# Optimization experiments

Measured on AMD Instinct MI355X. Metric: run time of the kernel, lower is better.

Reference implementation:

```python
import jax, jax.numpy as jnp
import numpy as np

THRESH = 0.5
LENS = 0.5
DECAY = 0.5
IN_SIZE = 8
T = 784 // IN_SIZE  # 98 timesteps
H = 1024
OUT = 10
SKIP = (2, 3, 4)
N_BATCH = 1024


@jax.custom_vjp
def act_fun(x):
    return (x > THRESH).astype(x.dtype)

def _af_fwd(x):
    return act_fun(x), x

def _af_bwd(x, g):
    return (g * (jnp.abs(x - THRESH) < LENS).astype(g.dtype),)

act_fun.defvjp(_af_fwd, _af_bwd)


def _make_mask(dim, cycle):
    base = np.array([1 if t % cycle == 0 else 0 for t in range(T)], dtype=np.int32)
    return np.stack([np.roll(base, n) for n in range(dim)])  # [dim, T]


def setup_inputs() -> dict:
    key = jax.random.key(0)
    ks = jax.random.split(key, 9)
    inp = {
        "input": jax.random.uniform(ks[0], (N_BATCH, 784), dtype=jnp.float32),
        "W1": jax.random.normal(ks[1], (H, IN_SIZE), dtype=jnp.float32) * 0.1,
        "b1": jax.random.normal(ks[2], (H,), dtype=jnp.float32) * 0.01,
        "W2": jax.random.normal(ks[3], (H, H), dtype=jnp.float32) * 0.03,
        "b2": jax.random.normal(ks[4], (H,), dtype=jnp.float32) * 0.01,
        "W3": jax.random.normal(ks[5], (H, H), dtype=jnp.float32) * 0.03,
        "b3": jax.random.normal(ks[6], (H,), dtype=jnp.float32) * 0.01,
        "W4": jax.random.normal(ks[7], (OUT, H), dtype=jnp.float32) * 0.03,
        "b4": jax.random.normal(ks[8], (OUT,), dtype=jnp.float32) * 0.01,
        "mask1": jnp.asarray(_make_mask(H, SKIP[0])),
        "mask2": jnp.asarray(_make_mask(H, SKIP[1])),
        "mask3": jnp.asarray(_make_mask(H, SKIP[2])),
    }
    return inp


def _gather_steps(x):
    # Faithful replication of the original (buggy) slicing: start = step*IN_SIZE,
    # but if start >= T - IN_SIZE the model uses the LAST IN_SIZE pixels.
    starts = np.array([s * IN_SIZE if s * IN_SIZE < T - IN_SIZE else 784 - IN_SIZE
                       for s in range(T)])
    idx = starts[:, None] + np.arange(IN_SIZE)  # [T, IN_SIZE]
    return jnp.transpose(x[:, idx], (1, 0, 2))  # [T, N, IN_SIZE]


def reference(input, W1, b1, W2, b2, W3, b3, W4, b4, mask1, mask2, mask3):
    N = input.shape[0]
    xs = _gather_steps(input)            # [T, N, IN_SIZE]
    mk1 = mask1.T                         # [T, H]
    mk2 = mask2.T
    mk3 = mask3.T

    def upd(drive, mem, spike, mk):
        mkf = mk.astype(mem.dtype)
        new_mem = mem * DECAY * (1.0 - spike) + drive
        mem = jnp.where(mk == 0, mem, new_mem)
        spike = act_fun(mem) * mkf
        return mem, spike

    zeros = lambda d: jnp.zeros((N, d), dtype=input.dtype)
    carry0 = (zeros(H), zeros(H), zeros(H), zeros(H), zeros(H), zeros(H),
              jnp.zeros((N, OUT), dtype=input.dtype), zeros(H), zeros(H), zeros(H))

    def step(carry, inp):
        m1, s1, m2, s2, m3, s3, osum, ss1, ss2, ss3 = carry
        x, k1, k2, k3 = inp
        m1, s1 = upd(x @ W1.T + b1, m1, s1, k1)
        m2, s2 = upd(s1 @ W2.T + b2, m2, s2, k2)
        m3, s3 = upd(s2 @ W3.T + b3, m3, s3, k3)
        out = s3 @ W4.T + b4
        return (m1, s1, m2, s2, m3, s3, osum + out,
                ss1 + s1, ss2 + s2, ss3 + s3), None

    carry, _ = jax.lax.scan(step, carry0, (xs, mk1, mk2, mk3))
    _, _, _, _, _, _, osum, ss1, ss2, ss3 = carry

    tw = jnp.asarray(T, dtype=input.dtype)
    outputs = osum / tw
    denom = jnp.asarray(N * H * T, dtype=input.dtype)
    layer_fr = jnp.stack([ss1.sum() / denom, ss2.sum() / denom, ss3.sum() / denom])
    hidden_spk = (ss1 / tw, ss2 / tw, ss3 / tw)
    return outputs, hidden_spk, layer_fr
```

## Files before the change

kernel.cpp:

```cpp
#include <hip/hip_runtime.h>

#define TTL 98
#define OUTD 10

typedef float f16v __attribute__((ext_vector_type(16)));
typedef short short8 __attribute__((ext_vector_type(8)));
typedef unsigned long ul2 __attribute__((ext_vector_type(2)));
typedef unsigned short ushort;

constexpr size_t MM = 1048576;
constexpr size_t OFF_OSUM = 5 * MM;
constexpr size_t OFF_XT   = OFF_OSUM + 10240;
constexpr size_t OFF_S1B  = OFF_XT + 802816;
constexpr size_t OFF_S2B  = OFF_S1B + 1605632;
constexpr size_t OFF_S1BT = OFF_S2B + 1103872;
constexpr size_t OFF_S2BT = OFF_S1BT + 1605632;
constexpr size_t OFF_W2S  = OFF_S2BT + 1103872;
constexpr size_t OFF_W3S  = OFF_W2S + 1572864;
constexpr size_t FIX_END  = OFF_W3S + 1585152;

constexpr size_t TAB_IDX2 = 0;
constexpr size_t TAB_IDX3 = 37632;
constexpr size_t TAB_CQ3  = 269696;
constexpr size_t TAB_L2   = 304192;
constexpr size_t TAB_L3   = 337984;

constexpr size_t AW3_PER_T = 168960;

__device__ inline void split3(float w, ushort& h, ushort& m, ushort& l) {
    unsigned u = __float_as_uint(w);
    h = (ushort)(u >> 16);
    float r1 = w - __uint_as_float(u & 0xFFFF0000u);
    unsigned u1 = __float_as_uint(r1);
    m = (ushort)(u1 >> 16);
    float r2 = r1 - __uint_as_float(u1 & 0xFFFF0000u);
    l = (ushort)(__float_as_uint(r2) >> 16);
}

__device__ inline short8 expand8(unsigned x) {
    union { unsigned u[4]; short8 v; } r;
#pragma unroll
    for (int q = 0; q < 4; ++q) {
        unsigned b = x >> (2 * q);
        r.u[q] = ((b & 1u) * 0x3F80u) | ((b & 2u) ? 0x3F800000u : 0u);
    }
    return r.v;
}

__device__ inline short8 ldsAF(const ushort* base) {
    union { unsigned long u[2]; short8 s; } r;
    r.u[0] = *(const unsigned long*)(base);
    r.u[1] = *(const unsigned long*)(base + 4);
    return r.s;
}
__device__ inline void ldsWR(ushort* dst, ul2 v) {
    *(unsigned long*)(dst) = v[0];
    *(unsigned long*)(dst + 4) = v[1];
}
#define ASOFF(cur, pi, row, col) (((((cur)*3 + (pi))*64 + (row))*36) + (col))

__global__ __launch_bounds__(256) void kSplit(
    const float* __restrict__ W2, const float* __restrict__ W3,
    ushort* __restrict__ W2S, ushort* __restrict__ W3S)
{
    int id = blockIdx.x * 256 + threadIdx.x;
    if (id < 1048576) {
        int p = id >> 19, rem = id & 524287, i = rem >> 9, q = rem & 511;
        ushort h, m, l;
        split3(W2[i * 1024 + 2 * q + p], h, m, l);
        size_t base = (size_t)p * 524288 + (size_t)i * 512 + q;
        W2S[base] = h; W2S[base + 1048576] = m; W2S[base + 2097152] = l;
    } else {
        int id2 = id - 1048576;
        if (id2 >= 1056768) return;
        int c = id2 / 352256, rem = id2 % 352256, i = rem / 344, q = rem % 344;
        int j = c + 3 * q;
        float w = (j < 1024) ? W3[i * 1024 + j] : 0.f;
        ushort h, m, l;
        split3(w, h, m, l);
        W3S[id2] = h; W3S[id2 + 1056768] = m; W3S[id2 + 2113536] = l;
    }
}

__global__ __launch_bounds__(256) void kPrep(const float* __restrict__ input,
                                             float* __restrict__ xT)
{
    __shared__ float Ls[64][65];
    int bx = blockIdx.x, tid = threadIdx.x;
    int wt = bx >> 4, nt = bx & 15;
    int w0 = wt * 64, n0 = nt * 64;
#pragma unroll
    for (int j = 0; j < 16; ++j) {
        int flat = tid + 256 * j;
        int a = flat >> 6, c = flat & 63;
        Ls[a][c] = (w0 + c < 784) ? input[(size_t)(n0 + a) * 784 + w0 + c] : 0.f;
    }
    __syncthreads();
#pragma unroll
    for (int j = 0; j < 16; ++j) {
        int flat = tid + 256 * j;
        int ii = flat >> 6, nn = flat & 63;
        if (w0 + ii < 784) xT[(size_t)(w0 + ii) * 1024 + n0 + nn] = Ls[nn][ii];
    }
}

__global__ __launch_bounds__(256) void kL1(
    const float* __restrict__ xT, const float* __restrict__ W1,
    const float* __restrict__ b1,
    unsigned long long* __restrict__ s1bits, float* __restrict__ ss1)
{
    int tid = threadIdx.x;
    int waveId = (blockIdx.x << 2) + (tid >> 6);
    int lane = tid & 63;
    int rowg = waveId >> 4;
    int nblk = waveId & 15;
    int i0 = rowg << 2;
    int n = (nblk << 6) + lane;
    float w[4][8], bb[4], mem[4], cnt[4];
#pragma unroll
    for (int r = 0; r < 4; ++r) {
#pragma unroll
        for (int e = 0; e < 8; ++e) w[r][e] = W1[(i0 + r) * 8 + e];
        bb[r] = b1[i0 + r]; mem[r] = 0.f; cnt[r] = 0.f;
    }
    float x[8], xn[8];
#pragma unroll
    for (int e = 0; e < 8; ++e) x[e] = xT[(size_t)e * 1024 + n];
    for (int t = 0; t < 12; ++t) {
        int st1 = ((t + 1) * 8 < TTL - 8) ? (t + 1) * 8 : (784 - 8);
#pragma unroll
        for (int e = 0; e < 8; ++e) xn[e] = xT[(size_t)(st1 + e) * 1024 + n];
#pragma unroll
        for (int r = 0; r < 4; ++r) {
            if (((t ^ (i0 + r)) & 1) == 0) {
                float d = bb[r];
#pragma unroll
                for (int e = 0; e < 8; ++e) d += w[r][e] * x[e];
                float m = mem[r] * 0.5f + d;
                mem[r] = m;
                bool sp = m > 0.5f;
                unsigned long long bm = __ballot(sp);
                if (lane == 0) s1bits[(size_t)(t * 512 + ((i0 + r) >> 1)) * 16 + nblk] = bm;
                if (sp) cnt[r] += 1.f;
            }
        }
#pragma unroll
        for (int e = 0; e < 8; ++e) x[e] = xn[e];
    }
    float dd[4];
#pragma unroll
    for (int r = 0; r < 4; ++r) {
        float d = bb[r];
#pragma unroll
        for (int e = 0; e < 8; ++e) d += w[r][e] * x[e];
        dd[r] = d;
    }
#pragma unroll 1
    for (int t = 12; t < TTL; t += 2) {
#pragma unroll
        for (int h = 0; h < 2; ++h) {
#pragma unroll
            for (int rr = 0; rr < 2; ++rr) {
                int r = h + rr * 2;
                float m = mem[r] * 0.5f + dd[r];
                mem[r] = m;
                bool sp = m > 0.5f;
                unsigned long long bm = __ballot(sp);
                if (lane == 0) s1bits[(size_t)((t + h) * 512 + ((i0 + r) >> 1)) * 16 + nblk] = bm;
                if (sp) cnt[r] += 1.f;
            }
        }
    }
#pragma unroll
    for (int r = 0; r < 4; ++r) ss1[(size_t)(i0 + r) * 1024 + n] = cnt[r];
}

__global__ __launch_bounds__(256) void kTab2(
    int* __restrict__ idx2, int* __restrict__ idx3, int* __restrict__ cq3)
{
    __shared__ int f2[256], f3[256];
    __shared__ int sidx2[384], sidx3[320];
    int t = blockIdx.x, tid = threadIdx.x;
    int a2[4], a3[4];
    int l2 = 0, l3 = 0;
#pragma unroll
    for (int e = 0; e < 4; ++e) {
        int i = tid * 4 + e;
        int u = (t - i) % TTL; if (u < 0) u += TTL;
        a2[e] = (u % 3 == 0); a3[e] = (u % 4 == 0);
        l2 += a2[e]; l3 += a3[e];
    }
    f2[tid] = l2; f3[tid] = l3;
    __syncthreads();
    for (int s = 1; s < 256; s <<= 1) {
        int v2 = (tid >= s) ? f2[tid - s] : 0;
        int v3 = (tid >= s) ? f3[tid - s] : 0;
        __syncthreads();
        f2[tid] += v2; f3[tid] += v3;
        __syncthreads();
    }
    int o2 = f2[tid] - l2, o3 = f3[tid] - l3;
    int c2 = f2[255], c3 = f3[255];
#pragma unroll
    for (int e = 0; e < 4; ++e) {
        int i = tid * 4 + e;
        if (a2[e]) { sidx2[o2] = i; ++o2; }
        if (a3[e]) { sidx3[o3] = i; ++o3; }
    }
    __syncthreads();
    for (int k = tid; k < 384; k += 256) idx2[t * 384 + k] = (k < c2) ? sidx2[k] : -1;
    for (int k = tid; k < 320; k += 256) idx3[t * 320 + k] = (k < c3) ? sidx3[k] : -1;
    for (int k = tid; k < 352; k += 256) {
        int j = (k < c2) ? sidx2[k] : 0;
        cq3[t * 352 + k] = (j % 3) * 352256 + j / 3;
    }
}

template<int C, int NACT>
__global__ __launch_bounds__(256) void kListCF(int* __restrict__ list)
{
    int flat = blockIdx.x * 256 + threadIdx.x;
    if (flat >= 1024 * NACT) return;
    int i = flat / NACT, s = flat % NACT;
    int ri = i % 98;
    int k0 = (98 - ri + C - 1) / C;
    int kw = NACT - k0; if (kw < 0) kw = 0;
    int t = (s < kw) ? (ri + (k0 + s) * C - 98) : (ri + (s - kw) * C);
    int rk = 0;
    int r = t;
#pragma unroll
    for (int k = 0; k < NACT; ++k) {
        rk += (r < i) ? (i - r + 97) / 98 : 0;
        r -= C; if (r < 0) r += 98;
    }
    list[i * NACT + s] = (t << 10) | rk;
}

template<int K>
__global__ __launch_bounds__(256) void kXb(const unsigned* __restrict__ in,
                                           unsigned* __restrict__ out, int t0)
{
    constexpr int Kw = K / 32;
    __shared__ unsigned L[1024];
    int bx = blockIdx.x, tid = threadIdx.x;
    int tt = t0 + bx / Kw, kw = bx % Kw;
    const unsigned* ip = in + ((size_t)tt * K + kw * 32) * 32;
#pragma unroll
    for (int g = 0; g < 4; ++g) L[g * 256 + tid] = ip[g * 256 + tid];
    __syncthreads();
    unsigned* op = out + ((size_t)tt * Kw + kw) * 1024;
#pragma unroll
    for (int g = 0; g < 4; ++g) {
        int n = g * 256 + tid;
        int w = n >> 5, b = n & 31;
        unsigned acc = 0;
#pragma unroll
        for (int k = 0; k < 32; ++k) acc |= ((L[k * 32 + w] >> b) & 1u) << k;
        op[n] = acc;
    }
}

__global__ __launch_bounds__(256) void kXbG3A(
    const unsigned* __restrict__ s2b, unsigned* __restrict__ s2bT,
    const ushort* __restrict__ Ws, const int* __restrict__ idx3,
    const int* __restrict__ cq3, ushort* __restrict__ AW3, int t0)
{
    __shared__ unsigned L[1024];
    int bx = blockIdx.x, tid = threadIdx.x;
    int tloc = bx / 66, r66 = bx % 66;
    int t = t0 + tloc;
    if (r66 < 11) {
        int kw = r66;
        const unsigned* ip = s2b + ((size_t)t * 352 + kw * 32) * 32;
#pragma unroll
        for (int g = 0; g < 4; ++g) L[g * 256 + tid] = ip[g * 256 + tid];
        __syncthreads();
        unsigned* op = s2bT + ((size_t)t * 11 + kw) * 1024;
#pragma unroll
        for (int g = 0; g < 4; ++g) {
            int n = g * 256 + tid;
            int w = n >> 5, b = n & 31;
            unsigned acc = 0;
#pragma unroll
            for (int k = 0; k < 32; ++k) acc |= ((L[k * 32 + w] >> b) & 1u) << k;
            op[n] = acc;
        }
    } else {
        int blk = r66 - 11;
        int flat = blk * 256 + tid;
        int r = flat / 44, kg = flat % 44;
        int k0 = kg * 8;
        int v = idx3[t * 320 + r];
        int i = v < 0 ? 0 : v;
        const int* cq = cq3 + t * 352 + k0;
        int c0 = cq[0], c1 = cq[1], c2 = cq[2], c3 = cq[3],
            c4 = cq[4], c5 = cq[5], c6 = cq[6], c7 = cq[7];
        size_t ia = (size_t)i * 344;
#pragma unroll
        for (int pi = 0; pi < 3; ++pi) {
            const ushort* wp = Ws + (size_t)pi * 1056768 + ia;
            union { ushort us[8]; ul2 v2; } o;
            o.us[0] = wp[c0]; o.us[1] = wp[c1]; o.us[2] = wp[c2]; o.us[3] = wp[c3];
            o.us[4] = wp[c4]; o.us[5] = wp[c5]; o.us[6] = wp[c6]; o.us[7] = wp[c7];
            *(ul2*)(AW3 + ((size_t)tloc * 3 + pi) * 112640 + (size_t)r * 352 + k0) = o.v2;
        }
    }
}


__device__ __forceinline__ void gm2_body(
    int bx, int tid, ushort* AsR,
    const ushort* __restrict__ Ws, const unsigned* __restrict__ s1bT,
    const int* __restrict__ idx2, float* __restrict__ drive, int t0)
{
    int tloc = bx / 24, rem = bx % 24;
    int mt = rem >> 2, nt4 = rem & 3;
    int t = t0 + tloc;
    int p = t & 1;
    int r0 = mt * 64, n0 = nt4 * 256;
    int ar = tid >> 2, ak8 = (tid & 3) * 8;
    int vR = idx2[t * 384 + r0 + ar];
    const ushort* Wrow = Ws + (size_t)p * 524288 + (size_t)(vR < 0 ? 0 : vR) * 512 + ak8;
    int wv = tid >> 6, lane = tid & 63;
    int mrow = lane & 31, kh8 = (lane >> 5) * 8;
    int nb = n0 + wv * 64 + mrow;
    f16v acc[2][2];
#pragma unroll
    for (int a = 0; a < 2; ++a)
#pragma unroll
        for (int b = 0; b < 2; ++b) acc[a][b] = (f16v)(0.f);

    ul2 c0r[3];
#pragma unroll
    for (int pi = 0; pi < 3; ++pi) c0r[pi] = *(const ul2*)(Wrow + (size_t)pi * 1048576);
#pragma unroll
    for (int pi = 0; pi < 3; ++pi) ldsWR(&AsR[ASOFF(0, pi, ar, ak8)], c0r[pi]);
    ul2 nxt[3];
#pragma unroll
    for (int pi = 0; pi < 3; ++pi) nxt[pi] = *(const ul2*)(Wrow + (size_t)pi * 1048576 + 32);
    unsigned w4c[2];
#pragma unroll
    for (int jj = 0; jj < 2; ++jj) w4c[jj] = s1bT[(size_t)t * 16 * 1024 + nb + jj * 32];
    __syncthreads();

    int cur = 0;
    for (int kc = 0; kc < 512; kc += 32) {
        if (kc + 32 < 512) {
#pragma unroll
            for (int pi = 0; pi < 3; ++pi) ldsWR(&AsR[ASOFF(cur ^ 1, pi, ar, ak8)], nxt[pi]);
        }
        unsigned w4n[2];
        if (kc + 32 < 512) {
#pragma unroll
            for (int jj = 0; jj < 2; ++jj)
                w4n[jj] = s1bT[((size_t)t * 16 + ((kc + 32) >> 5)) * 1024 + nb + jj * 32];
        }
        ul2 n2[3];
        if (kc + 64 < 512) {
#pragma unroll
            for (int pi = 0; pi < 3; ++pi)
                n2[pi] = *(const ul2*)(Wrow + (size_t)pi * 1048576 + kc + 64);
        }
#pragma unroll
        for (int s2 = 0; s2 < 2; ++s2) {
            int kcol = s2 * 16 + kh8;
            short8 bf[2];
#pragma unroll
            for (int jj = 0; jj < 2; ++jj) bf[jj] = expand8((w4c[jj] >> kcol) & 0xFFu);
#pragma unroll
            for (int wr2 = 0; wr2 < 2; ++wr2) {
                short8 af0 = ldsAF(&AsR[ASOFF(cur, 0, wr2 * 32 + mrow, kcol)]);
                short8 af1 = ldsAF(&AsR[ASOFF(cur, 1, wr2 * 32 + mrow, kcol)]);
                short8 af2 = ldsAF(&AsR[ASOFF(cur, 2, wr2 * 32 + mrow, kcol)]);
#pragma unroll
                for (int jj = 0; jj < 2; ++jj) {
                    acc[wr2][jj] = __builtin_amdgcn_mfma_f32_32x32x16_bf16(af2, bf[jj], acc[wr2][jj], 0, 0, 0);
                    acc[wr2][jj] = __builtin_amdgcn_mfma_f32_32x32x16_bf16(af1, bf[jj], acc[wr2][jj], 0, 0, 0);
                    acc[wr2][jj] = __builtin_amdgcn_mfma_f32_32x32x16_bf16(af0, bf[jj], acc[wr2][jj], 0, 0, 0);
                }
            }
        }
        __syncthreads();
        cur ^= 1;
        nxt[0] = n2[0]; nxt[1] = n2[1]; nxt[2] = n2[2];
        w4c[0] = w4n[0]; w4c[1] = w4n[1];
    }
#pragma unroll
    for (int wr2 = 0; wr2 < 2; ++wr2)
#pragma unroll
        for (int jj = 0; jj < 2; ++jj)
#pragma unroll
            for (int reg = 0; reg < 16; ++reg) {
                int rowl = r0 + wr2 * 32 + (reg & 3) + 8 * (reg >> 2) + 4 * (lane >> 5);
                drive[((size_t)tloc * 384 + rowl) * 1024 + nb + jj * 32] = acc[wr2][jj][reg];
            }
}

__device__ __forceinline__ void gm3_body(
    int bx, int tid, ushort* AsR,
    const ushort* __restrict__ AW3, const unsigned* __restrict__ s2bT,
    float* __restrict__ drive, int t0)
{
    int tloc = bx / 20, rem = bx % 20;
    int mt = rem >> 2, nt4 = rem & 3;
    int t = t0 + tloc;
    int r0 = mt * 64, n0 = nt4 * 256;
    int ar = tid >> 2, ak8 = (tid & 3) * 8;
    const ushort* Ab = AW3 + (size_t)tloc * 337920 + (size_t)(r0 + ar) * 352 + ak8;
    int wv = tid >> 6, lane = tid & 63;
    int mrow = lane & 31, kh8 = (lane >> 5) * 8;
    int nb = n0 + wv * 64 + mrow;
    f16v acc[2][2];
#pragma unroll
    for (int a = 0; a < 2; ++a)
#pragma unroll
        for (int b = 0; b < 2; ++b) acc[a][b] = (f16v)(0.f);

    ul2 c0r[3];
#pragma unroll
    for (int pi = 0; pi < 3; ++pi) c0r[pi] = *(const ul2*)(Ab + (size_t)pi * 112640);
#pragma unroll
    for (int pi = 0; pi < 3; ++pi) ldsWR(&AsR[ASOFF(0, pi, ar, ak8)], c0r[pi]);
    ul2 nxt[3];
#pragma unroll
    for (int pi = 0; pi < 3; ++pi) nxt[pi] = *(const ul2*)(Ab + (size_t)pi * 112640 + 32);
    unsigned w4c[2];
#pragma unroll
    for (int jj = 0; jj < 2; ++jj) w4c[jj] = s2bT[(size_t)t * 11 * 1024 + nb + jj * 32];
    __syncthreads();

    int cur = 0;
    for (int kc = 0; kc < 352; kc += 32) {
        if (kc + 32 < 352) {
#pragma unroll
            for (int pi = 0; pi < 3; ++pi) ldsWR(&AsR[ASOFF(cur ^ 1, pi, ar, ak8)], nxt[pi]);
        }
        unsigned w4n[2];
        if (kc + 32 < 352) {
#pragma unroll
            for (int jj = 0; jj < 2; ++jj)
                w4n[jj] = s2bT[((size_t)t * 11 + ((kc + 32) >> 5)) * 1024 + nb + jj * 32];
        }
        ul2 n2[3];
        if (kc + 64 < 352) {
#pragma unroll
            for (int pi = 0; pi < 3; ++pi)
                n2[pi] = *(const ul2*)(Ab + (size_t)pi * 112640 + kc + 64);
        }
#pragma unroll
        for (int s2 = 0; s2 < 2; ++s2) {
            int kcol = s2 * 16 + kh8;
            short8 bf[2];
#pragma unroll
            for (int jj = 0; jj < 2; ++jj) bf[jj] = expand8((w4c[jj] >> kcol) & 0xFFu);
#pragma unroll
            for (int wr2 = 0; wr2 < 2; ++wr2) {
                short8 af0 = ldsAF(&AsR[ASOFF(cur, 0, wr2 * 32 + mrow, kcol)]);
                short8 af1 = ldsAF(&AsR[ASOFF(cur, 1, wr2 * 32 + mrow, kcol)]);
                short8 af2 = ldsAF(&AsR[ASOFF(cur, 2, wr2 * 32 + mrow, kcol)]);
#pragma unroll
                for (int jj = 0; jj < 2; ++jj) {
                    acc[wr2][jj] = __builtin_amdgcn_mfma_f32_32x32x16_bf16(af2, bf[jj], acc[wr2][jj], 0, 0, 0);
                    acc[wr2][jj] = __builtin_amdgcn_mfma_f32_32x32x16_bf16(af1, bf[jj], acc[wr2][jj], 0, 0, 0);
                    acc[wr2][jj] = __builtin_amdgcn_mfma_f32_32x32x16_bf16(af0, bf[jj], acc[wr2][jj], 0, 0, 0);
                }
            }
        }
        __syncthreads();
        cur ^= 1;
        nxt[0] = n2[0]; nxt[1] = n2[1]; nxt[2] = n2[2];
        w4c[0] = w4n[0]; w4c[1] = w4n[1];
    }
#pragma unroll
    for (int wr2 = 0; wr2 < 2; ++wr2)
#pragma unroll
        for (int jj = 0; jj < 2; ++jj)
#pragma unroll
            for (int reg = 0; reg < 16; ++reg) {
                int rowl = r0 + wr2 * 32 + (reg & 3) + 8 * (reg >> 2) + 4 * (lane >> 5);
                drive[((size_t)tloc * 320 + rowl) * 1024 + nb + jj * 32] = acc[wr2][jj][reg];
            }
}

__global__ __launch_bounds__(256) void kGM2K(
    const ushort* __restrict__ Ws, const unsigned* __restrict__ s1bT,
    const int* __restrict__ idx2, float* __restrict__ drive, int t0)
{
    __shared__ ushort AsR[2 * 3 * 64 * 36];
    gm2_body(blockIdx.x, threadIdx.x, AsR, Ws, s1bT, idx2, drive, t0);
}
__global__ __launch_bounds__(256) void kGM3K(
    const ushort* __restrict__ AW3, const unsigned* __restrict__ s2bT,
    float* __restrict__ drive, int t0)
{
    __shared__ ushort AsR[2 * 3 * 64 * 36];
    gm3_body(blockIdx.x, threadIdx.x, AsR, AW3, s2bT, drive, t0);
}

__global__ __launch_bounds__(256) void kGMF(
    const ushort* __restrict__ W2S, const unsigned* __restrict__ s1bT,
    const int* __restrict__ idx2, float* __restrict__ drv2, int t0_2, int n2blocks,
    const ushort* __restrict__ AW3, const unsigned* __restrict__ s2bT,
    float* __restrict__ drv3, int t0_3)
{
    __shared__ ushort AsR[2 * 3 * 64 * 36];
    int bx = blockIdx.x;
    if (bx < n2blocks) gm2_body(bx, threadIdx.x, AsR, W2S, s1bT, idx2, drv2, t0_2);
    else               gm3_body(bx - n2blocks, threadIdx.x, AsR, AW3, s2bT, drv3, t0_3);
}

template<int MP, int KBP, bool BITS, int NACT>
__device__ __forceinline__ void rk_body(
    int bx, int tid,
    const float* __restrict__ drive, const float* __restrict__ bias,
    const int* __restrict__ list,
    float* __restrict__ mG, float* __restrict__ ssG,
    unsigned long long* __restrict__ bitsOut, int t0, int nt)
{
    int row = bx >> 2;
    int wv  = ((bx & 3) << 2) + (tid >> 6);
    int lane = tid & 63;
    int n = (wv << 6) + lane;
    size_t idx = (size_t)row * 1024 + n;
    float mv = mG[idx];
    float cnt = 0.f;
    float bv = bias[row];
    const int* lp = list + row * NACT;
    int t1 = t0 + nt;
    int s0 = 0;
    while (s0 < NACT && (lp[s0] >> 10) < t0) ++s0;
    int s1 = s0;
    while (s1 < NACT && (lp[s1] >> 10) < t1) ++s1;
    if (s0 < s1) {
        int v0 = lp[s0];
        float d0 = drive[((size_t)((v0 >> 10) - t0) * MP + (v0 & 1023)) * 1024 + n];
        int v1 = 0; float d1 = 0.f;
        if (s0 + 1 < s1) {
            v1 = lp[s0 + 1];
            d1 = drive[((size_t)((v1 >> 10) - t0) * MP + (v1 & 1023)) * 1024 + n];
        }
        for (int s = s0; s < s1; ++s) {
            int vc = v0;
            float dcur = d0;
            v0 = v1; d0 = d1;
            if (s + 2 < s1) {
                v1 = lp[s + 2];
                d1 = drive[((size_t)((v1 >> 10) - t0) * MP + (v1 & 1023)) * 1024 + n];
            }
            float d = dcur + bv;
            float m = mv * 0.5f + d;
            mv = m;
            bool sp = m > 0.5f;
            if (BITS) {
                unsigned long long bm = __ballot(sp);
                if (lane == 0) bitsOut[((size_t)(vc >> 10) * KBP + (vc & 1023)) * 16 + wv] = bm;
            }
            cnt += sp ? 1.f : 0.f;
        }
    }
    mG[idx] = mv;
    ssG[idx] += cnt;
}

template<int MP, int KBP, bool BITS, int NACT>
__global__ __launch_bounds__(256) void kRK(
    const float* __restrict__ drive, const float* __restrict__ bias,
    const int* __restrict__ list,
    float* __restrict__ mG, float* __restrict__ ssG,
    unsigned long long* __restrict__ bitsOut, int t0, int nt)
{
    rk_body<MP, KBP, BITS, NACT>(blockIdx.x, threadIdx.x, drive, bias, list,
                                 mG, ssG, bitsOut, t0, nt);
}

__global__ __launch_bounds__(256) void kRKF(
    const float* __restrict__ drv3, const float* __restrict__ b3,
    const int* __restrict__ list3, float* __restrict__ m3, float* __restrict__ ss3,
    int t0_3, int nt3,
    const float* __restrict__ drv2, const float* __restrict__ b2,
    const int* __restrict__ list2, float* __restrict__ m2, float* __restrict__ ss2,
    unsigned long long* __restrict__ s2bits, int t0_2, int nt2)
{
    int bx = blockIdx.x;
    if (bx < 4096)
        rk_body<320, 0, false, 25>(bx, threadIdx.x, drv3, b3, list3, m3, ss3,
                                   nullptr, t0_3, nt3);
    else
        rk_body<384, 352, true, 33>(bx - 4096, threadIdx.x, drv2, b2, list2, m2, ss2,
                                    s2bits, t0_2, nt2);
}

__global__ __launch_bounds__(256) void kTail(
    const float* __restrict__ ssBase, const float* __restrict__ W4,
    float* __restrict__ osum, float* __restrict__ out, float* __restrict__ fr)
{
    int bx = blockIdx.x, tid = threadIdx.x;
    if (bx < 768) {
        __shared__ float Ls[64][65];
        __shared__ float red[4];
        int l = bx >> 8;
        int tile = bx & 255;
        int i0 = (tile >> 4) * 64, n0 = (tile & 15) * 64;
        const float* ss = ssBase + (size_t)l * MM;
        float* o = out + 10240 + (size_t)l * MM;
        float sum = 0.f;
#pragma unroll
        for (int j = 0; j < 16; ++j) {
            int flat = tid + 256 * j;
            int a = flat >> 6, c = flat & 63;
            float v = ss[(size_t)(i0 + a) * 1024 + n0 + c];
            Ls[a][c] = v;
            sum += v;
        }
        __syncthreads();
        for (int off = 32; off > 0; off >>= 1) sum += __shfl_down(sum, off, 64);
        if ((tid & 63) == 0) red[tid >> 6] = sum;
        __syncthreads();
        if (tid == 0) {
            float s = red[0] + red[1] + red[2] + red[3];
            atomicAdd(&fr[l], s * (1.0f / (1024.0f * 1024.0f * 98.0f)));
        }
#pragma unroll
        for (int j = 0; j < 16; ++j) {
            int flat = tid + 256 * j;
            int nn = flat >> 6, ii = flat & 63;
            o[(size_t)(n0 + nn) * 1024 + i0 + ii] = Ls[ii][nn] * (1.0f / 98.0f);
        }
    } else {
        int b = bx - 768;
        int ks = b >> 4, nt = b & 15;
        int n = nt * 64 + (tid & 63);
        int og = tid >> 6;
        const float* ss3 = ssBase + (size_t)2 * MM;
        float a0 = 0.f, a1 = 0.f, a2 = 0.f;
        int k0 = ks * 256;
        for (int k = k0; k < k0 + 256; ++k) {
            float v = ss3[(size_t)k * 1024 + n];
            a0 += v * W4[og * 1024 + k];
            a1 += v * W4[(og + 4) * 1024 + k];
            if (og < 2) a2 += v * W4[(og + 8) * 1024 + k];
        }
        atomicAdd(&osum[n * OUTD + og], a0);
        atomicAdd(&osum[n * OUTD + og + 4], a1);
        if (og < 2) atomicAdd(&osum[n * OUTD + og + 8], a2);
    }
}

__global__ void kOut(const float* __restrict__ osum, const float* __restrict__ b4,
                     float* __restrict__ out)
{
    int idx = blockIdx.x * 256 + threadIdx.x;
    if (idx < 1024 * OUTD) out[idx] = osum[idx] * (1.0f / 98.0f) + b4[idx % OUTD];
}

extern "C" void kernel_launch(void* const* d_in, const int* in_sizes, int n_in,
                              void* d_out, int out_size, void* d_ws, size_t ws_size,
                              hipStream_t stream)
{
    const float* input = (const float*)d_in[0];
    const float* W1    = (const float*)d_in[1];
    const float* b1    = (const float*)d_in[2];
    const float* W2    = (const float*)d_in[3];
    const float* b2    = (const float*)d_in[4];
    const float* W3    = (const float*)d_in[5];
    const float* b3    = (const float*)d_in[6];
    const float* W4    = (const float*)d_in[7];
    const float* b4    = (const float*)d_in[8];

    float* ws = (float*)d_ws;
    float* ss1  = ws;
    float* ss2  = ws + MM;
    float* ss3  = ws + 2 * MM;
    float* m2   = ws + 3 * MM;
    float* m3   = ws + 4 * MM;
    float* osum = ws + OFF_OSUM;
    float* xT   = ws + OFF_XT;
    int*   tabs = (int*)(ws + OFF_XT);
    int* idx2  = tabs + TAB_IDX2;
    int* idx3  = tabs + TAB_IDX3;
    int* cq3   = tabs + TAB_CQ3;
    int* list2 = tabs + TAB_L2;
    int* list3 = tabs + TAB_L3;
    unsigned int* s1b  = (unsigned int*)(ws + OFF_S1B);
    unsigned int* s2b  = (unsigned int*)(ws + OFF_S2B);
    unsigned int* s1bT = (unsigned int*)(ws + OFF_S1BT);
    unsigned int* s2bT = (unsigned int*)(ws + OFF_S2BT);
    ushort* W2S = (ushort*)(ws + OFF_W2S);
    ushort* W3S = (ushort*)(ws + OFF_W3S);
    float* out  = (float*)d_out;

    size_t availF = ws_size / sizeof(float);
    constexpr size_t PER_T = AW3_PER_T + 384 * 1024 + 320 * 1024;
    int tc = 10;
    const int cands[8] = {98, 66, 49, 40, 33, 25, 14, 10};
    for (int ci = 0; ci < 8; ++ci) {
        if (FIX_END + (size_t)cands[ci] * PER_T <= availF) { tc = cands[ci]; break; }
    }
    ushort* AW3 = (ushort*)(ws + FIX_END);
    float* drv2 = ws + FIX_END + (size_t)tc * AW3_PER_T;
    float* drv3 = drv2 + (size_t)tc * 384 * 1024;

    hipMemsetAsync(ws, 0, (5 * MM + 10240) * sizeof(float), stream);
    hipMemsetAsync(s2b, 0, 1103872 * sizeof(unsigned int), stream);
    hipMemsetAsync(out + 3155968, 0, 3 * sizeof(float), stream);

    kSplit<<<8224, 256, 0, stream>>>(W2, W3, W2S, W3S);
    kPrep<<<208, 256, 0, stream>>>(input, xT);
    kL1<<<1024, 256, 0, stream>>>(xT, W1, b1, (unsigned long long*)s1b, ss1);
    kTab2<<<98, 256, 0, stream>>>(idx2, idx3, cq3);
    kListCF<3, 33><<<132, 256, 0, stream>>>(list2);
    kListCF<4, 25><<<100, 256, 0, stream>>>(list3);
    kXb<512><<<1568, 256, 0, stream>>>(s1b, s1bT, 0);

    int nc = (TTL + tc - 1) / tc;
    auto ntOf = [&](int c) { int t0c = c * tc; return (TTL - t0c < tc) ? (TTL - t0c) : tc; };

    kGM2K<<<ntOf(0) * 24, 256, 0, stream>>>(W2S, s1bT, idx2, drv2, 0);
    kRK<384, 352, true, 33><<<4096, 256, 0, stream>>>(drv2, b2, list2, m2, ss2,
                                                      (unsigned long long*)s2b, 0, ntOf(0));
    kXbG3A<<<ntOf(0) * 66, 256, 0, stream>>>(s2b, s2bT, W3S, idx3, cq3, AW3, 0);

    for (int c = 0; c + 1 < nc; ++c) {
        int t03 = c * tc, t02 = (c + 1) * tc;
        int n2b = ntOf(c + 1) * 24, n3b = ntOf(c) * 20;
        kGMF<<<n2b + n3b, 256, 0, stream>>>(W2S, s1bT, idx2, drv2, t02, n2b,
                                            AW3, s2bT, drv3, t03);
        kRKF<<<8192, 256, 0, stream>>>(drv3, b3, list3, m3, ss3, t03, ntOf(c),
                                       drv2, b2, list2, m2, ss2,
                                       (unsigned long long*)s2b, t02, ntOf(c + 1));
        kXbG3A<<<ntOf(c + 1) * 66, 256, 0, stream>>>(s2b, s2bT, W3S, idx3, cq3, AW3, t02);
    }
    int cl = nc - 1, t0l = cl * tc;
    kGM3K<<<ntOf(cl) * 20, 256, 0, stream>>>(AW3, s2bT, drv3, t0l);
    kRK<320, 0, false, 25><<<4096, 256, 0, stream>>>(drv3, b3, list3, m3, ss3,
                                                     nullptr, t0l, ntOf(cl));

    kTail<<<832, 256, 0, stream>>>(ss1, W4, osum, out, out + 3155968);
    kOut<<<40, 256, 0, stream>>>(osum, b4, out);
}
```

Measured before the change: 518.7 us.

## Load MFMA A-fragments directly from global memory, dropping LDS staging

The two spiking-layer GEMM bodies no longer stage the weight (A) tiles through double-buffered shared memory with a __syncthreads per K-chunk. Each lane now loads its own MFMA A fragments straight from global memory into registers and prefetches the next chunk. This removes the LDS traffic, the barriers and the LDS footprint, which may raise occupancy. In exchange, the four waves of a block each reload the same A rows (4x global/L2 traffic), and register pressure rises from holding 24 short8 fragments.

```diff
diff --git a/kernel.cpp b/kernel.cpp
--- a/kernel.cpp
+++ b/kernel.cpp
@@ -46,18 +46,6 @@
     }
     return r.v;
 }
-
-__device__ inline short8 ldsAF(const ushort* base) {
-    union { unsigned long u[2]; short8 s; } r;
-    r.u[0] = *(const unsigned long*)(base);
-    r.u[1] = *(const unsigned long*)(base + 4);
-    return r.s;
-}
-__device__ inline void ldsWR(ushort* dst, ul2 v) {
-    *(unsigned long*)(dst) = v[0];
-    *(unsigned long*)(dst + 4) = v[1];
-}
-#define ASOFF(cur, pi, row, col) (((((cur)*3 + (pi))*64 + (row))*36) + (col))
 
 __global__ __launch_bounds__(256) void kSplit(
     const float* __restrict__ W2, const float* __restrict__ W3,
@@ -309,7 +297,7 @@
 
 
 __device__ __forceinline__ void gm2_body(
-    int bx, int tid, ushort* AsR,
+    int bx, int tid,
     const ushort* __restrict__ Ws, const unsigned* __restrict__ s1bT,
     const int* __restrict__ idx2, float* __restrict__ drive, int t0)
 {
@@ -318,48 +306,47 @@
     int t = t0 + tloc;
     int p = t & 1;
     int r0 = mt * 64, n0 = nt4 * 256;
-    int ar = tid >> 2, ak8 = (tid & 3) * 8;
-    int vR = idx2[t * 384 + r0 + ar];
-    const ushort* Wrow = Ws + (size_t)p * 524288 + (size_t)(vR < 0 ? 0 : vR) * 512 + ak8;
     int wv = tid >> 6, lane = tid & 63;
     int mrow = lane & 31, kh8 = (lane >> 5) * 8;
     int nb = n0 + wv * 64 + mrow;
+    int vR0 = idx2[t * 384 + r0 + mrow];
+    int vR1 = idx2[t * 384 + r0 + 32 + mrow];
+    const ushort* Ar[2];
+    Ar[0] = Ws + (size_t)p * 524288 + (size_t)(vR0 < 0 ? 0 : vR0) * 512 + kh8;
+    Ar[1] = Ws + (size_t)p * 524288 + (size_t)(vR1 < 0 ? 0 : vR1) * 512 + kh8;
     f16v acc[2][2];
 #pragma unroll
     for (int a = 0; a < 2; ++a)
 #pragma unroll
         for (int b = 0; b < 2; ++b) acc[a][b] = (f16v)(0.f);
 
-    ul2 c0r[3];
-#pragma unroll
-    for (int pi = 0; pi < 3; ++pi) c0r[pi] = *(const ul2*)(Wrow + (size_t)pi * 1048576);
-#pragma unroll
-    for (int pi = 0; pi < 3; ++pi) ldsWR(&AsR[ASOFF(0, pi, ar, ak8)], c0r[pi]);
-    ul2 nxt[3];
-#pragma unroll
-    for (int pi = 0; pi < 3; ++pi) nxt[pi] = *(const ul2*)(Wrow + (size_t)pi * 1048576 + 32);
+    short8 fc[2][2][3];
+#pragma unroll
+    for (int s2 = 0; s2 < 2; ++s2)
+#pragma unroll
+        for (int wr2 = 0; wr2 < 2; ++wr2)
+#pragma unroll
+            for (int pi = 0; pi < 3; ++pi)
+                fc[s2][wr2][pi] = *(const short8*)(Ar[wr2] + (size_t)pi * 1048576 + s2 * 16);
     unsigned w4c[2];
 #pragma unroll
     for (int jj = 0; jj < 2; ++jj) w4c[jj] = s1bT[(size_t)t * 16 * 1024 + nb + jj * 32];
-    __syncthreads();
-
-    int cur = 0;
+
+#pragma unroll 1
     for (int kc = 0; kc < 512; kc += 32) {
-        if (kc + 32 < 512) {
-#pragma unroll
-            for (int pi = 0; pi < 3; ++pi) ldsWR(&AsR[ASOFF(cur ^ 1, pi, ar, ak8)], nxt[pi]);
-        }
+        short8 fn[2][2][3];
         unsigned w4n[2];
         if (kc + 32 < 512) {
 #pragma unroll
+            for (int s2 = 0; s2 < 2; ++s2)
+#pragma unroll
+                for (int wr2 = 0; wr2 < 2; ++wr2)
+#pragma unroll
+                    for (int pi = 0; pi < 3; ++pi)
+                        fn[s2][wr2][pi] = *(const short8*)(Ar[wr2] + (size_t)pi * 1048576 + kc + 32 + s2 * 16);
+#pragma unroll
             for (int jj = 0; jj < 2; ++jj)
                 w4n[jj] = s1bT[((size_t)t * 16 + ((kc + 32) >> 5)) * 1024 + nb + jj * 32];
-        }
-        ul2 n2[3];
-        if (kc + 64 < 512) {
-#pragma unroll
-            for (int pi = 0; pi < 3; ++pi)
-                n2[pi] = *(const ul2*)(Wrow + (size_t)pi * 1048576 + kc + 64);
         }
 #pragma unroll
         for (int s2 = 0; s2 < 2; ++s2) {
@@ -369,20 +356,20 @@
             for (int jj = 0; jj < 2; ++jj) bf[jj] = expand8((w4c[jj] >> kcol) & 0xFFu);
 #pragma unroll
             for (int wr2 = 0; wr2 < 2; ++wr2) {
-                short8 af0 = ldsAF(&AsR[ASOFF(cur, 0, wr2 * 32 + mrow, kcol)]);
-                short8 af1 = ldsAF(&AsR[ASOFF(cur, 1, wr2 * 32 + mrow, kcol)]);
-                short8 af2 = ldsAF(&AsR[ASOFF(cur, 2, wr2 * 32 + mrow, kcol)]);
 #pragma unroll
                 for (int jj = 0; jj < 2; ++jj) {
-                    acc[wr2][jj] = __builtin_amdgcn_mfma_f32_32x32x16_bf16(af2, bf[jj], acc[wr2][jj], 0, 0, 0);
-                    acc[wr2][jj] = __builtin_amdgcn_mfma_f32_32x32x16_bf16(af1, bf[jj], acc[wr2][jj], 0, 0, 0);
-                    acc[wr2][jj] = __builtin_amdgcn_mfma_f32_32x32x16_bf16(af0, bf[jj], acc[wr2][jj], 0, 0, 0);
+                    acc[wr2][jj] = __builtin_amdgcn_mfma_f32_32x32x16_bf16(fc[s2][wr2][2], bf[jj], acc[wr2][jj], 0, 0, 0);
+                    acc[wr2][jj] = __builtin_amdgcn_mfma_f32_32x32x16_bf16(fc[s2][wr2][1], bf[jj], acc[wr2][jj], 0, 0, 0);
+                    acc[wr2][jj] = __builtin_amdgcn_mfma_f32_32x32x16_bf16(fc[s2][wr2][0], bf[jj], acc[wr2][jj], 0, 0, 0);
                 }
             }
         }
-        __syncthreads();
-        cur ^= 1;
-        nxt[0] = n2[0]; nxt[1] = n2[1]; nxt[2] = n2[2];
+#pragma unroll
+        for (int s2 = 0; s2 < 2; ++s2)
+#pragma unroll
+            for (int wr2 = 0; wr2 < 2; ++wr2)
+#pragma unroll
+                for (int pi = 0; pi < 3; ++pi) fc[s2][wr2][pi] = fn[s2][wr2][pi];
         w4c[0] = w4n[0]; w4c[1] = w4n[1];
     }
 #pragma unroll
@@ -397,7 +384,7 @@
 }
 
 __device__ __forceinline__ void gm3_body(
-    int bx, int tid, ushort* AsR,
+    int bx, int tid,
     const ushort* __restrict__ AW3, const unsigned* __restrict__ s2bT,
     float* __restrict__ drive, int t0)
 {
@@ -405,47 +392,45 @@
     int mt = rem >> 2, nt4 = rem & 3;
     int t = t0 + tloc;
     int r0 = mt * 64, n0 = nt4 * 256;
-    int ar = tid >> 2, ak8 = (tid & 3) * 8;
-    const ushort* Ab = AW3 + (size_t)tloc * 337920 + (size_t)(r0 + ar) * 352 + ak8;
     int wv = tid >> 6, lane = tid & 63;
     int mrow = lane & 31, kh8 = (lane >> 5) * 8;
     int nb = n0 + wv * 64 + mrow;
+    const ushort* Ar[2];
+    Ar[0] = AW3 + (size_t)tloc * 337920 + (size_t)(r0 + mrow) * 352 + kh8;
+    Ar[1] = AW3 + (size_t)tloc * 337920 + (size_t)(r0 + 32 + mrow) * 352 + kh8;
     f16v acc[2][2];
 #pragma unroll
     for (int a = 0; a < 2; ++a)
 #pragma unroll
         for (int b = 0; b < 2; ++b) acc[a][b] = (f16v)(0.f);
 
-    ul2 c0r[3];
-#pragma unroll
-    for (int pi = 0; pi < 3; ++pi) c0r[pi] = *(const ul2*)(Ab + (size_t)pi * 112640);
-#pragma unroll
-    for (int pi = 0; pi < 3; ++pi) ldsWR(&AsR[ASOFF(0, pi, ar, ak8)], c0r[pi]);
-    ul2 nxt[3];
-#pragma unroll
-    for (int pi = 0; pi < 3; ++pi) nxt[pi] = *(const ul2*)(Ab + (size_t)pi * 112640 + 32);
+    short8 fc[2][2][3];
+#pragma unroll
+    for (int s2 = 0; s2 < 2; ++s2)
+#pragma unroll
+        for (int wr2 = 0; wr2 < 2; ++wr2)
+#pragma unroll
+            for (int pi = 0; pi < 3; ++pi)
+                fc[s2][wr2][pi] = *(const short8*)(Ar[wr2] + (size_t)pi * 112640 + s2 * 16);
     unsigned w4c[2];
 #pragma unroll
     for (int jj = 0; jj < 2; ++jj) w4c[jj] = s2bT[(size_t)t * 11 * 1024 + nb + jj * 32];
-    __syncthreads();
-
-    int cur = 0;
+
+#pragma unroll 1
     for (int kc = 0; kc < 352; kc += 32) {
-        if (kc + 32 < 352) {
-#pragma unroll
-            for (int pi = 0; pi < 3; ++pi) ldsWR(&AsR[ASOFF(cur ^ 1, pi, ar, ak8)], nxt[pi]);
-        }
+        short8 fn[2][2][3];
         unsigned w4n[2];
         if (kc + 32 < 352) {
 #pragma unroll
+            for (int s2 = 0; s2 < 2; ++s2)
+#pragma unroll
+                for (int wr2 = 0; wr2 < 2; ++wr2)
+#pragma unroll
+                    for (int pi = 0; pi < 3; ++pi)
+                        fn[s2][wr2][pi] = *(const short8*)(Ar[wr2] + (size_t)pi * 112640 + kc + 32 + s2 * 16);
+#pragma unroll
             for (int jj = 0; jj < 2; ++jj)
                 w4n[jj] = s2bT[((size_t)t * 11 + ((kc + 32) >> 5)) * 1024 + nb + jj * 32];
-        }
-        ul2 n2[3];
-        if (kc + 64 < 352) {
-#pragma unroll
-            for (int pi = 0; pi < 3; ++pi)
-                n2[pi] = *(const ul2*)(Ab + (size_t)pi * 112640 + kc + 64);
         }
 #pragma unroll
         for (int s2 = 0; s2 < 2; ++s2) {
@@ -455,20 +440,20 @@
             for (int jj = 0; jj < 2; ++jj) bf[jj] = expand8((w4c[jj] >> kcol) & 0xFFu);
 #pragma unroll
             for (int wr2 = 0; wr2 < 2; ++wr2) {
-                short8 af0 = ldsAF(&AsR[ASOFF(cur, 0, wr2 * 32 + mrow, kcol)]);
-                short8 af1 = ldsAF(&AsR[ASOFF(cur, 1, wr2 * 32 + mrow, kcol)]);
-                short8 af2 = ldsAF(&AsR[ASOFF(cur, 2, wr2 * 32 + mrow, kcol)]);
 #pragma unroll
                 for (int jj = 0; jj < 2; ++jj) {
-                    acc[wr2][jj] = __builtin_amdgcn_mfma_f32_32x32x16_bf16(af2, bf[jj], acc[wr2][jj], 0, 0, 0);
-                    acc[wr2][jj] = __builtin_amdgcn_mfma_f32_32x32x16_bf16(af1, bf[jj], acc[wr2][jj], 0, 0, 0);
-                    acc[wr2][jj] = __builtin_amdgcn_mfma_f32_32x32x16_bf16(af0, bf[jj], acc[wr2][jj], 0, 0, 0);
+                    acc[wr2][jj] = __builtin_amdgcn_mfma_f32_32x32x16_bf16(fc[s2][wr2][2], bf[jj], acc[wr2][jj], 0, 0, 0);
+                    acc[wr2][jj] = __builtin_amdgcn_mfma_f32_32x32x16_bf16(fc[s2][wr2][1], bf[jj], acc[wr2][jj], 0, 0, 0);
+                    acc[wr2][jj] = __builtin_amdgcn_mfma_f32_32x32x16_bf16(fc[s2][wr2][0], bf[jj], acc[wr2][jj], 0, 0, 0);
                 }
             }
         }
-        __syncthreads();
-        cur ^= 1;
-        nxt[0] = n2[0]; nxt[1] = n2[1]; nxt[2] = n2[2];
+#pragma unroll
+        for (int s2 = 0; s2 < 2; ++s2)
+#pragma unroll
+            for (int wr2 = 0; wr2 < 2; ++wr2)
+#pragma unroll
+                for (int pi = 0; pi < 3; ++pi) fc[s2][wr2][pi] = fn[s2][wr2][pi];
         w4c[0] = w4n[0]; w4c[1] = w4n[1];
     }
 #pragma unroll
@@ -486,15 +471,13 @@
     const ushort* __restrict__ Ws, const unsigned* __restrict__ s1bT,
     const int* __restrict__ idx2, float* __restrict__ drive, int t0)
 {
-    __shared__ ushort AsR[2 * 3 * 64 * 36];
-    gm2_body(blockIdx.x, threadIdx.x, AsR, Ws, s1bT, idx2, drive, t0);
+    gm2_body(blockIdx.x, threadIdx.x, Ws, s1bT, idx2, drive, t0);
 }
 __global__ __launch_bounds__(256) void kGM3K(
     const ushort* __restrict__ AW3, const unsigned* __restrict__ s2bT,
     float* __restrict__ drive, int t0)
 {
-    __shared__ ushort AsR[2 * 3 * 64 * 36];
-    gm3_body(blockIdx.x, threadIdx.x, AsR, AW3, s2bT, drive, t0);
+    gm3_body(blockIdx.x, threadIdx.x, AW3, s2bT, drive, t0);
 }
 
 __global__ __launch_bounds__(256) void kGMF(
@@ -503,10 +486,9 @@
     const ushort* __restrict__ AW3, const unsigned* __restrict__ s2bT,
     float* __restrict__ drv3, int t0_3)
 {
-    __shared__ ushort AsR[2 * 3 * 64 * 36];
     int bx = blockIdx.x;
-    if (bx < n2blocks) gm2_body(bx, threadIdx.x, AsR, W2S, s1bT, idx2, drv2, t0_2);
-    else               gm3_body(bx - n2blocks, threadIdx.x, AsR, AW3, s2bT, drv3, t0_3);
+    if (bx < n2blocks) gm2_body(bx, threadIdx.x, W2S, s1bT, idx2, drv2, t0_2);
+    else               gm3_body(bx - n2blocks, threadIdx.x, AW3, s2bT, drv3, t0_3);
 }
 
 template<int MP, int KBP, bool BITS, int NACT>
```

Measured after the change: 676.2 us. +30.4%, slower.

## Re-pipeline chunk stages into two fused kernels per chunk, cap chunk size

Applied to the files above, without the earlier changes.

Reorganizes the per-chunk schedule so each iteration launches two fused kernels. One runs the layer-3 GEMM alongside the layer-2 recurrence. The other runs the next layer-2 GEMM, the layer-3 recurrence and the spike transpose/gather together. This cuts the launches per chunk from three to two and lets independent stages from different chunks share one grid. The chunk-size candidates are limited to 25/14/10, which increases the number of chunks for finer-grained pipelining. That in turn adds more launches overall and more block-type divergence within each fused grid.

```diff
diff --git a/kernel.cpp b/kernel.cpp
--- a/kernel.cpp
+++ b/kernel.cpp
@@ -260,13 +260,12 @@
     }
 }
 
-__global__ __launch_bounds__(256) void kXbG3A(
+__device__ __forceinline__ void xbg3a_body(
+    int bx, int tid, unsigned* L,
     const unsigned* __restrict__ s2b, unsigned* __restrict__ s2bT,
     const ushort* __restrict__ Ws, const int* __restrict__ idx3,
     const int* __restrict__ cq3, ushort* __restrict__ AW3, int t0)
 {
-    __shared__ unsigned L[1024];
-    int bx = blockIdx.x, tid = threadIdx.x;
     int tloc = bx / 66, r66 = bx % 66;
     int t = t0 + tloc;
     if (r66 < 11) {
@@ -480,33 +479,6 @@
                 int rowl = r0 + wr2 * 32 + (reg & 3) + 8 * (reg >> 2) + 4 * (lane >> 5);
                 drive[((size_t)tloc * 320 + rowl) * 1024 + nb + jj * 32] = acc[wr2][jj][reg];
             }
-}
-
-__global__ __launch_bounds__(256) void kGM2K(
-    const ushort* __restrict__ Ws, const unsigned* __restrict__ s1bT,
-    const int* __restrict__ idx2, float* __restrict__ drive, int t0)
-{
-    __shared__ ushort AsR[2 * 3 * 64 * 36];
-    gm2_body(blockIdx.x, threadIdx.x, AsR, Ws, s1bT, idx2, drive, t0);
-}
-__global__ __launch_bounds__(256) void kGM3K(
-    const ushort* __restrict__ AW3, const unsigned* __restrict__ s2bT,
-    float* __restrict__ drive, int t0)
-{
-    __shared__ ushort AsR[2 * 3 * 64 * 36];
-    gm3_body(blockIdx.x, threadIdx.x, AsR, AW3, s2bT, drive, t0);
-}
-
-__global__ __launch_bounds__(256) void kGMF(
-    const ushort* __restrict__ W2S, const unsigned* __restrict__ s1bT,
-    const int* __restrict__ idx2, float* __restrict__ drv2, int t0_2, int n2blocks,
-    const ushort* __restrict__ AW3, const unsigned* __restrict__ s2bT,
-    float* __restrict__ drv3, int t0_3)
-{
-    __shared__ ushort AsR[2 * 3 * 64 * 36];
-    int bx = blockIdx.x;
-    if (bx < n2blocks) gm2_body(bx, threadIdx.x, AsR, W2S, s1bT, idx2, drv2, t0_2);
-    else               gm3_body(bx - n2blocks, threadIdx.x, AsR, AW3, s2bT, drv3, t0_3);
 }
 
 template<int MP, int KBP, bool BITS, int NACT>
@@ -562,6 +534,14 @@
     ssG[idx] += cnt;
 }
 
+__global__ __launch_bounds__(256) void kGM2K(
+    const ushort* __restrict__ Ws, const unsigned* __restrict__ s1bT,
+    const int* __restrict__ idx2, float* __restrict__ drive, int t0)
+{
+    __shared__ ushort AsR[2 * 3 * 64 * 36];
+    gm2_body(blockIdx.x, threadIdx.x, AsR, Ws, s1bT, idx2, drive, t0);
+}
+
 template<int MP, int KBP, bool BITS, int NACT>
 __global__ __launch_bounds__(256) void kRK(
     const float* __restrict__ drive, const float* __restrict__ bias,
@@ -573,21 +553,38 @@
                                  mG, ssG, bitsOut, t0, nt);
 }
 
-__global__ __launch_bounds__(256) void kRKF(
-    const float* __restrict__ drv3, const float* __restrict__ b3,
-    const int* __restrict__ list3, float* __restrict__ m3, float* __restrict__ ss3,
-    int t0_3, int nt3,
+__global__ __launch_bounds__(256) void kF1(
+    const ushort* __restrict__ AW3, const unsigned* __restrict__ s2bT,
+    float* __restrict__ drv3, int t0_3, int n3b,
     const float* __restrict__ drv2, const float* __restrict__ b2,
     const int* __restrict__ list2, float* __restrict__ m2, float* __restrict__ ss2,
     unsigned long long* __restrict__ s2bits, int t0_2, int nt2)
 {
+    __shared__ ushort AsR[2 * 3 * 64 * 36];
     int bx = blockIdx.x;
-    if (bx < 4096)
-        rk_body<320, 0, false, 25>(bx, threadIdx.x, drv3, b3, list3, m3, ss3,
-                                   nullptr, t0_3, nt3);
-    else
-        rk_body<384, 352, true, 33>(bx - 4096, threadIdx.x, drv2, b2, list2, m2, ss2,
-                                    s2bits, t0_2, nt2);
+    if (bx < n3b) gm3_body(bx, threadIdx.x, AsR, AW3, s2bT, drv3, t0_3);
+    else rk_body<384, 352, true, 33>(bx - n3b, threadIdx.x, drv2, b2, list2,
+                                     m2, ss2, s2bits, t0_2, nt2);
+}
+
+__global__ __launch_bounds__(256) void kF2(
+    const ushort* __restrict__ W2S, const unsigned* __restrict__ s1bT,
+    const int* __restrict__ idx2, float* __restrict__ drv2, int t0_2, int n2b,
+    const float* __restrict__ drv3, const float* __restrict__ b3,
+    const int* __restrict__ list3, float* __restrict__ m3, float* __restrict__ ss3,
+    int t0_3, int nt3, int nrk3,
+    const unsigned* __restrict__ s2b, unsigned* __restrict__ s2bT,
+    const ushort* __restrict__ W3S, const int* __restrict__ idx3,
+    const int* __restrict__ cq3, ushort* __restrict__ AW3, int t0_x)
+{
+    __shared__ ushort AsR[2 * 3 * 64 * 36];
+    int bx = blockIdx.x;
+    if (bx < n2b) { gm2_body(bx, threadIdx.x, AsR, W2S, s1bT, idx2, drv2, t0_2); return; }
+    bx -= n2b;
+    if (bx < nrk3) { rk_body<320, 0, false, 25>(bx, threadIdx.x, drv3, b3, list3,
+                                                m3, ss3, nullptr, t0_3, nt3); return; }
+    bx -= nrk3;
+    xbg3a_body(bx, threadIdx.x, (unsigned*)AsR, s2b, s2bT, W3S, idx3, cq3, AW3, t0_x);
 }
 
 __global__ __launch_bounds__(256) void kTail(
@@ -692,8 +689,8 @@
     size_t availF = ws_size / sizeof(float);
     constexpr size_t PER_T = AW3_PER_T + 384 * 1024 + 320 * 1024;
     int tc = 10;
-    const int cands[8] = {98, 66, 49, 40, 33, 25, 14, 10};
-    for (int ci = 0; ci < 8; ++ci) {
+    const int cands[3] = {25, 14, 10};
+    for (int ci = 0; ci < 3; ++ci) {
         if (FIX_END + (size_t)cands[ci] * PER_T <= availF) { tc = cands[ci]; break; }
     }
     ushort* AW3 = (ushort*)(ws + FIX_END);
@@ -718,22 +715,26 @@
     kGM2K<<<ntOf(0) * 24, 256, 0, stream>>>(W2S, s1bT, idx2, drv2, 0);
     kRK<384, 352, true, 33><<<4096, 256, 0, stream>>>(drv2, b2, list2, m2, ss2,
                                                       (unsigned long long*)s2b, 0, ntOf(0));
-    kXbG3A<<<ntOf(0) * 66, 256, 0, stream>>>(s2b, s2bT, W3S, idx3, cq3, AW3, 0);
-
-    for (int c = 0; c + 1 < nc; ++c) {
-        int t03 = c * tc, t02 = (c + 1) * tc;
-        int n2b = ntOf(c + 1) * 24, n3b = ntOf(c) * 20;
-        kGMF<<<n2b + n3b, 256, 0, stream>>>(W2S, s1bT, idx2, drv2, t02, n2b,
-                                            AW3, s2bT, drv3, t03);
-        kRKF<<<8192, 256, 0, stream>>>(drv3, b3, list3, m3, ss3, t03, ntOf(c),
-                                       drv2, b2, list2, m2, ss2,
-                                       (unsigned long long*)s2b, t02, ntOf(c + 1));
-        kXbG3A<<<ntOf(c + 1) * 66, 256, 0, stream>>>(s2b, s2bT, W3S, idx3, cq3, AW3, t02);
-    }
-    int cl = nc - 1, t0l = cl * tc;
-    kGM3K<<<ntOf(cl) * 20, 256, 0, stream>>>(AW3, s2bT, drv3, t0l);
-    kRK<320, 0, false, 25><<<4096, 256, 0, stream>>>(drv3, b3, list3, m3, ss3,
-                                                     nullptr, t0l, ntOf(cl));
+    {
+        int n2b = (nc > 1) ? ntOf(1) * 24 : 0;
+        int nxb = ntOf(0) * 66;
+        kF2<<<n2b + nxb, 256, 0, stream>>>(W2S, s1bT, idx2, drv2, tc, n2b,
+                                           drv3, b3, list3, m3, ss3, 0, 0, 0,
+                                           s2b, s2bT, W3S, idx3, cq3, AW3, 0);
+    }
+    for (int i = 0; i < nc; ++i) {
+        int n3b = ntOf(i) * 20;
+        int nt2 = (i + 1 < nc) ? ntOf(i + 1) : 0;
+        kF1<<<n3b + (nt2 ? 4096 : 0), 256, 0, stream>>>(
+            AW3, s2bT, drv3, i * tc, n3b,
+            drv2, b2, list2, m2, ss2, (unsigned long long*)s2b, (i + 1) * tc, nt2);
+        int n2b = (i + 2 < nc) ? ntOf(i + 2) * 24 : 0;
+        int nxb = (i + 1 < nc) ? ntOf(i + 1) * 66 : 0;
+        kF2<<<n2b + 4096 + nxb, 256, 0, stream>>>(
+            W2S, s1bT, idx2, drv2, (i + 2) * tc, n2b,
+            drv3, b3, list3, m3, ss3, i * tc, ntOf(i), 4096,
+            s2b, s2bT, W3S, idx3, cq3, AW3, (i + 1) * tc);
+    }
 
     kTail<<<832, 256, 0, stream>>>(ss1, W4, osum, out, out + 3155968);
     kOut<<<40, 256, 0, stream>>>(osum, b4, out);
```

Result: slower. 624.7 us (+20.4%).
